# Kernel optimization log

Hardware: AMD Instinct MI355X
Metric: run time of the kernel (lower is better)

## Reference

```python
import jax, jax.numpy as jnp
import numpy as np

L = 3          # num_layers
D = 512        # hidden_dim
B, N = 8, 1024
EPS = 1e-5


def layernorm(x, gamma, beta):
    mu = jnp.mean(x, axis=-1, keepdims=True)
    var = jnp.var(x, axis=-1, keepdims=True)
    return (x - mu) * jax.lax.rsqrt(var + EPS) * gamma + beta


def setup_inputs() -> dict:
    key = jax.random.key(0)
    ks = jax.random.split(key, 12)
    s = 1.0 / np.sqrt(D)
    node_features = jax.random.normal(ks[0], (B, N, D), dtype=jnp.float32)
    adjacency_matrix = jax.random.randint(ks[1], (B, N, N), 0, 2, dtype=jnp.int32)
    return {
        "node_features": node_features,
        "adjacency_matrix": adjacency_matrix,
        # attn_linear: Linear(2D, 1) -> weight [2D], bias scalar, per layer
        "attn_w": jax.random.normal(ks[2], (L, 2 * D), dtype=jnp.float32) * (1.0 / np.sqrt(2 * D)),
        "attn_b": jax.random.normal(ks[3], (L,), dtype=jnp.float32) * 0.01,
        "W1": jax.random.normal(ks[4], (L, D, 4 * D), dtype=jnp.float32) * s,
        "b1": jnp.zeros((L, 4 * D), dtype=jnp.float32),
        "W2": jax.random.normal(ks[5], (L, 4 * D, D), dtype=jnp.float32) * (1.0 / np.sqrt(4 * D)),
        "b2": jnp.zeros((L, D), dtype=jnp.float32),
        "g1": jnp.ones((L, D), dtype=jnp.float32),
        "beta1": jnp.zeros((L, D), dtype=jnp.float32),
        "g2": jnp.ones((L, D), dtype=jnp.float32),
        "beta2": jnp.zeros((L, D), dtype=jnp.float32),
    }


def reference(node_features, adjacency_matrix, attn_w, attn_b, W1, b1, W2, b2, g1, beta1, g2, beta2):
    n = adjacency_matrix.shape[-1]
    # adjacency + self loops; mask of allowed edges
    mask = (adjacency_matrix.astype(jnp.float32) + jnp.eye(n, dtype=jnp.float32)) > 0  # [B,N,N]
    x = node_features
    d = x.shape[-1]
    for l in range(attn_w.shape[0]):
        # score_ij = a1.h_i + a2.h_j + b  (== Linear(concat(h_i,h_j)))
        si = x @ attn_w[l, :d]           # [B,N]
        sj = x @ attn_w[l, d:]           # [B,N]
        scores = si[:, :, None] + sj[:, None, :] + attn_b[l]   # [B,N,N]
        scores = jnp.where(scores >= 0, scores, 0.2 * scores)  # LeakyReLU(0.2)
        scores = jnp.where(mask, scores, -jnp.inf)
        attn = jax.nn.softmax(scores, axis=-1)                  # diag always unmasked
        agg = jnp.einsum('bij,bjd->bid', attn, x)
        h = layernorm(x + agg, g1[l], beta1[l])
        ff = jax.nn.gelu(h @ W1[l] + b1[l], approximate=False) @ W2[l] + b2[l]
        x = layernorm(h + ff, g2[l], beta2[l])
    return x
```

## Files before the change

### kernel.cpp

```cpp
#include <hip/hip_runtime.h>
#include <math.h>

#define NB 8
#define NN 1024
#define DD 512

typedef unsigned short u16;
typedef unsigned int u32;
typedef unsigned long long u64;
typedef __attribute__((ext_vector_type(8))) short bfrag;
typedef __attribute__((ext_vector_type(4))) float ffrag;

__device__ __forceinline__ u16 f2b(float f) {
    union { float f; u32 u; } v; v.f = f;
    u32 r = v.u + 0x7fffu + ((v.u >> 16) & 1u);
    return (u16)(r >> 16);
}
__device__ __forceinline__ float b2f(u16 b) {
    union { u32 u; float f; } v; v.u = ((u32)b) << 16;
    return v.f;
}

__device__ __forceinline__ float gelu_cheap(float v) {
    float s = v * 0.70710678118654752f;
    float a = fabsf(s);
    float t = 1.0f / (1.0f + 0.3275911f * a);
    float p = ((((1.061405429f * t - 1.453152027f) * t + 1.421413741f) * t
                - 0.284496736f) * t + 0.254829592f) * t;
    float erfa = 1.0f - p * __expf(-a * a);
    float erfs = copysignf(erfa, s);
    return 0.5f * v * (1.0f + erfs);
}

__device__ __forceinline__ void gload_lds16(const void* g, void* l) {
    __builtin_amdgcn_global_load_lds(
        (const __attribute__((address_space(1))) void*)g,
        (__attribute__((address_space(3))) void*)l, 16, 0, 0);
}

__device__ __forceinline__ void tcvt_body(
    const float* __restrict__ in, u16* __restrict__ out,
    int R, int C, int r0, int c0, int t, float tile[32][33])
{
    int tr = t >> 3, tc = (t & 7) * 4;
    float4 v = *(const float4*)(in + (size_t)(r0 + tr) * C + c0 + tc);
    tile[tr][tc + 0] = v.x; tile[tr][tc + 1] = v.y;
    tile[tr][tc + 2] = v.z; tile[tr][tc + 3] = v.w;
    __syncthreads();
    u32 w0 = (u32)f2b(tile[tc + 0][tr]) | ((u32)f2b(tile[tc + 1][tr]) << 16);
    u32 w1 = (u32)f2b(tile[tc + 2][tr]) | ((u32)f2b(tile[tc + 3][tr]) << 16);
    uint2 wv; wv.x = w0; wv.y = w1;
    *(uint2*)(out + (size_t)(c0 + tr) * R + r0 + tc) = wv;
}

__global__ __launch_bounds__(256) void transpose_cvt(
    const float* __restrict__ in, u16* __restrict__ out,
    int R, int C, size_t inStr, size_t outStr)
{
    __shared__ float tile[32][33];
    int z = blockIdx.z;
    tcvt_body(in + inStr * z, out + outStr * z,
              R, C, blockIdx.y * 32, blockIdx.x * 32, threadIdx.x, tile);
}

__global__ __launch_bounds__(256) void prep_fused(
    const int* __restrict__ adj, u64* __restrict__ mb,
    const float* __restrict__ nf, const float* __restrict__ attn_w,
    float* __restrict__ si, float* __restrict__ sj, u16* __restrict__ xT)
{
    __shared__ float tile[32][33];
    int bid = blockIdx.x;
    int tid = threadIdx.x;
    if (bid < 512) {
        int idx = bid * 256 + tid;
        int w = idx & 15;
        int bi = idx >> 4;
        int i = bi & 1023;
        const int4* p = (const int4*)(adj + (size_t)bi * NN + w * 64);
        u64 m = 0;
#pragma unroll
        for (int q = 0; q < 16; ++q) {
            int4 v = p[q];
            if (v.x > 0) m |= 1ull << (q * 4 + 0);
            if (v.y > 0) m |= 1ull << (q * 4 + 1);
            if (v.z > 0) m |= 1ull << (q * 4 + 2);
            if (v.w > 0) m |= 1ull << (q * 4 + 3);
        }
        if (w == (i >> 6)) m |= 1ull << (i & 63);
        mb[idx] = m;
    } else if (bid < 2560) {
        int wave = tid >> 6;
        int lane = tid & 63;
        int row = (bid - 512) * 4 + wave;
        const float4* xr = (const float4*)(nf + (size_t)row * DD) + lane * 2;
        const float4* w1 = (const float4*)(attn_w) + lane * 2;
        const float4* w2 = (const float4*)(attn_w + DD) + lane * 2;
        float a = 0.f, b2 = 0.f;
#pragma unroll
        for (int c = 0; c < 2; ++c) {
            float4 xv = xr[c], wa = w1[c], wb = w2[c];
            a  += xv.x * wa.x + xv.y * wa.y + xv.z * wa.z + xv.w * wa.w;
            b2 += xv.x * wb.x + xv.y * wb.y + xv.z * wb.z + xv.w * wb.w;
        }
#pragma unroll
        for (int off = 32; off > 0; off >>= 1) {
            a  += __shfl_xor(a, off);
            b2 += __shfl_xor(b2, off);
        }
        if (lane == 0) { si[row] = a; sj[row] = b2; }
    } else {
        int q = bid - 2560;
        int bx = q & 15, by = (q >> 4) & 31, bz = q >> 9;
        tcvt_body(nf + (size_t)bz * NN * DD, xT + (size_t)bz * NN * DD,
                  1024, 512, by * 32, bx * 32, tid, tile);
    }
}

__global__ __launch_bounds__(256) void trans_w(
    const float* __restrict__ W1, const float* __restrict__ W2,
    u16* __restrict__ W1t, u16* __restrict__ W2t)
{
    __shared__ float tile[32][33];
    int z = blockIdx.z;
    int bx = blockIdx.x, by = blockIdx.y;
    if (z < 3) {
        tcvt_body(W1 + (size_t)z * 512 * 2048, W1t + (size_t)z * 1048576,
                  512, 2048, by * 32, bx * 32, threadIdx.x, tile);
    } else {
        int q = by * 64 + bx;
        int bx2 = q & 15, by2 = q >> 4;
        tcvt_body(W2 + (size_t)(z - 3) * 2048 * 512, W2t + (size_t)(z - 3) * 1048576,
                  2048, 512, by2 * 32, bx2 * 32, threadIdx.x, tile);
    }
}

__global__ __launch_bounds__(256) void softmax_p(
    const float* __restrict__ si, const float* __restrict__ sj,
    const float* __restrict__ attn_b, const u64* __restrict__ mb,
    u16* __restrict__ P)
{
    __shared__ u16 sb[8 * NN];
    int b  = blockIdx.x >> 7;
    int i0 = (blockIdx.x & 127) * 8;
    int tid = threadIdx.x;
    int r = tid >> 5, l32 = tid & 31;
    int i = i0 + r;
    float bb = attn_b[0];
    float siv = si[b * NN + i];
    const float* sjb = sj + b * NN;
    const u64* mbr = mb + ((size_t)b * NN + i) * 16;

    float sv[32];
    float mx = -INFINITY;
#pragma unroll
    for (int q = 0; q < 32; ++q) {
        int j = q * 32 + l32;
        u64 w = mbr[q >> 1];
        int bit = ((q & 1) << 5) + l32;
        float s = siv + sjb[j] + bb;
        s = (s >= 0.f) ? s : 0.2f * s;
        s = ((w >> bit) & 1ull) ? s : -INFINITY;
        sv[q] = s;
        mx = fmaxf(mx, s);
    }
#pragma unroll
    for (int off = 16; off > 0; off >>= 1) mx = fmaxf(mx, __shfl_xor(mx, off, 32));
    float sum = 0.f;
#pragma unroll
    for (int q = 0; q < 32; ++q) {
        float p = __expf(sv[q] - mx);
        sv[q] = p;
        sum += p;
    }
#pragma unroll
    for (int off = 16; off > 0; off >>= 1) sum += __shfl_xor(sum, off, 32);
    float inv = 1.f / sum;
#pragma unroll
    for (int q = 0; q < 32; ++q)
        sb[r * NN + q * 32 + l32] = f2b(sv[q] * inv);
    __syncthreads();
    const uint4* src = (const uint4*)sb;
    uint4* dst = (uint4*)(P + ((size_t)b * NN + i0) * NN);
#pragma unroll
    for (int t = 0; t < 4; ++t) dst[t * 256 + tid] = src[t * 256 + tid];
}

template <int EPI>
__global__ __launch_bounds__(256) void gemm64(
    const u16* __restrict__ A, const u16* __restrict__ Bm,
    const float* __restrict__ bias, const void* __restrict__ res,
    void* __restrict__ Cout, int K, int N, int lda, int ldb,
    size_t aStr, size_t bStr, size_t cStr, size_t resStr)
{
    __shared__ __align__(16) u16 lds[24576];
    int gx = gridDim.x, gy = gridDim.y;
    int wg = blockIdx.x + gx * (blockIdx.y + gy * blockIdx.z);
    int nwg = gx * gy * gridDim.z;
    wg = (wg & 7) * (nwg >> 3) + (wg >> 3);
    int z = wg / (gx * gy);
    int rem = wg - z * (gx * gy);
    int by = rem / gx, bx = rem - by * gx;
    int m0 = by * 64, n0 = bx * 128;
    int tid = threadIdx.x;
    int lane = tid & 63, wv = tid >> 6;

    const u16* ag[2]; const u16* bg[4];
    u32 la[2], lb[4];
#pragma unroll
    for (int i = 0; i < 2; ++i) {
        int q = i * 256 + tid;
        int row = q >> 3, c = q & 7;
        ag[i] = A + aStr * z + (size_t)(m0 + row) * lda + (c ^ (row & 7)) * 8;
        la[i] = i * 2048 + wv * 512;
    }
#pragma unroll
    for (int i = 0; i < 4; ++i) {
        int q = i * 256 + tid;
        int row = q >> 3, c = q & 7;
        bg[i] = Bm + bStr * z + (size_t)(n0 + row) * ldb + (c ^ (row & 7)) * 8;
        lb[i] = 8192 + i * 2048 + wv * 512;
    }

    int mw = (wv >> 1) * 32, nw = (wv & 1) * 64;
    int lr = lane & 15, lq = lane >> 4;
    int sw = lr & 7;

    ffrag acc[2][4];
#pragma unroll
    for (int i = 0; i < 2; ++i)
#pragma unroll
        for (int j = 0; j < 4; ++j) acc[i][j] = (ffrag){0.f, 0.f, 0.f, 0.f};

#pragma unroll
    for (int i = 0; i < 2; ++i) gload_lds16(ag[i], &lds[la[i]]);
#pragma unroll
    for (int i = 0; i < 4; ++i) gload_lds16(bg[i], &lds[lb[i]]);

    for (int k0 = 0; k0 < K; k0 += 64) {
        int cur = (k0 >> 6) & 1;
        if (k0 + 64 < K) {
#pragma unroll
            for (int i = 0; i < 2; ++i)
                gload_lds16(ag[i] + k0 + 64, &lds[((cur ^ 1) << 12) + la[i]]);
#pragma unroll
            for (int i = 0; i < 4; ++i)
                gload_lds16(bg[i] + k0 + 64, &lds[((cur ^ 1) << 13) + lb[i]]);
            asm volatile("s_waitcnt vmcnt(6)" ::: "memory");
        } else {
            asm volatile("s_waitcnt vmcnt(0)" ::: "memory");
        }
        asm volatile("s_barrier" ::: "memory");

        const u16* Ab = &lds[cur << 12];
        const u16* Bb = &lds[8192 + (cur << 13)];
#pragma unroll
        for (int h = 0; h < 2; ++h) {
            bfrag af[2], bf[4];
#pragma unroll
            for (int i = 0; i < 2; ++i)
                af[i] = *(const bfrag*)&Ab[(mw + i * 16 + lr) * 64 + ((h * 4 + lq) ^ sw) * 8];
#pragma unroll
            for (int j = 0; j < 4; ++j)
                bf[j] = *(const bfrag*)&Bb[(nw + j * 16 + lr) * 64 + ((h * 4 + lq) ^ sw) * 8];
#pragma unroll
            for (int i = 0; i < 2; ++i)
#pragma unroll
                for (int j = 0; j < 4; ++j)
                    acc[i][j] = __builtin_amdgcn_mfma_f32_16x16x32_bf16(af[i], bf[j], acc[i][j], 0, 0, 0);
        }
        asm volatile("s_waitcnt lgkmcnt(0)\ns_barrier" ::: "memory");
    }

    float* Cf = (float*)Cout + cStr * z;
    const float* resf = (const float*)res;
    const u16*   resb = (const u16*)res;
#pragma unroll
    for (int i = 0; i < 2; ++i) {
        int row = m0 + mw + i * 16 + lq * 4;
#pragma unroll
        for (int j = 0; j < 4; ++j) {
            int col = n0 + nw + j * 16 + lr;
            float bv = (EPI != 0) ? bias[col] : 0.f;
#pragma unroll
            for (int r = 0; r < 4; ++r) {
                float v = acc[i][j][r] + bv;
                size_t off = (size_t)(row + r) * N + col;
                if (EPI == 0) {
                    Cf[off] = v + resf[resStr * z + off];
                } else {
                    Cf[off] = v + b2f(resb[off]);
                }
            }
        }
    }
}

template <int EPI>
__global__ __launch_bounds__(256) void gemm128(
    const u16* __restrict__ A, const u16* __restrict__ Bm,
    const float* __restrict__ bias, const void* __restrict__ res,
    void* __restrict__ Cout, int K, int N, int lda, int ldb,
    size_t aStr, size_t bStr, size_t cStr, size_t resStr)
{
    __shared__ __align__(16) u16 lds[32768];
    int gx = gridDim.x, gy = gridDim.y;
    int wg = blockIdx.x + gx * (blockIdx.y + gy * blockIdx.z);
    int nwg = gx * gy * gridDim.z;
    wg = (wg & 7) * (nwg >> 3) + (wg >> 3);
    int z = wg / (gx * gy);
    int rem = wg - z * (gx * gy);
    int by = rem / gx, bx = rem - by * gx;
    int m0 = by * 128, n0 = bx * 128;
    int tid = threadIdx.x;
    int lane = tid & 63, wv = tid >> 6;

    const u16* ag[4]; const u16* bg[4];
    u32 la[4], lb[4];
#pragma unroll
    for (int i = 0; i < 4; ++i) {
        int q = i * 256 + tid;
        int row = q >> 3, c = q & 7;
        ag[i] = A + aStr * z + (size_t)(m0 + row) * lda + (c ^ (row & 7)) * 8;
        la[i] = i * 2048 + wv * 512;
        bg[i] = Bm + bStr * z + (size_t)(n0 + row) * ldb + (c ^ (row & 7)) * 8;
        lb[i] = 16384 + i * 2048 + wv * 512;
    }

    int mw = (wv >> 1) * 64, nw = (wv & 1) * 64;
    int lr = lane & 15, lq = lane >> 4;
    int sw = lr & 7;

    ffrag acc[4][4];
#pragma unroll
    for (int i = 0; i < 4; ++i)
#pragma unroll
        for (int j = 0; j < 4; ++j) acc[i][j] = (ffrag){0.f, 0.f, 0.f, 0.f};

#pragma unroll
    for (int i = 0; i < 4; ++i) gload_lds16(ag[i], &lds[la[i]]);
#pragma unroll
    for (int i = 0; i < 4; ++i) gload_lds16(bg[i], &lds[lb[i]]);

    for (int k0 = 0; k0 < K; k0 += 64) {
        int cur = (k0 >> 6) & 1;
        if (k0 + 64 < K) {
#pragma unroll
            for (int i = 0; i < 4; ++i)
                gload_lds16(ag[i] + k0 + 64, &lds[((cur ^ 1) << 13) + la[i]]);
#pragma unroll
            for (int i = 0; i < 4; ++i)
                gload_lds16(bg[i] + k0 + 64, &lds[((cur ^ 1) << 13) + lb[i]]);
            asm volatile("s_waitcnt vmcnt(8)" ::: "memory");
        } else {
            asm volatile("s_waitcnt vmcnt(0)" ::: "memory");
        }
        asm volatile("s_barrier" ::: "memory");

        const u16* Ab = &lds[cur << 13];
        const u16* Bb = &lds[16384 + (cur << 13)];
#pragma unroll
        for (int h = 0; h < 2; ++h) {
            bfrag af[4], bf[4];
#pragma unroll
            for (int i = 0; i < 4; ++i)
                af[i] = *(const bfrag*)&Ab[(mw + i * 16 + lr) * 64 + ((h * 4 + lq) ^ sw) * 8];
#pragma unroll
            for (int j = 0; j < 4; ++j)
                bf[j] = *(const bfrag*)&Bb[(nw + j * 16 + lr) * 64 + ((h * 4 + lq) ^ sw) * 8];
#pragma unroll
            for (int i = 0; i < 4; ++i)
#pragma unroll
                for (int j = 0; j < 4; ++j)
                    acc[i][j] = __builtin_amdgcn_mfma_f32_16x16x32_bf16(af[i], bf[j], acc[i][j], 0, 0, 0);
        }
        asm volatile("s_waitcnt lgkmcnt(0)\ns_barrier" ::: "memory");
    }

    float* Cf = (float*)Cout + cStr * z;
    u16*   Cb = (u16*)Cout + cStr * z;
    const float* resf = (const float*)res;
    const u16*   resb = (const u16*)res;
    if (EPI == 1) {
        u16* sb = lds;
#pragma unroll
        for (int i = 0; i < 4; ++i) {
            int rr = mw + i * 16 + lq * 4;
#pragma unroll
            for (int j = 0; j < 4; ++j) {
                int cc = nw + j * 16 + lr;
                float bv = bias[n0 + cc];
#pragma unroll
                for (int r = 0; r < 4; ++r)
                    sb[(rr + r) * 136 + cc] = f2b(gelu_cheap(acc[i][j][r] + bv));
            }
        }
        __syncthreads();
        u16* Crow = Cb + (size_t)m0 * N + n0;
#pragma unroll
        for (int t = 0; t < 8; ++t) {
            int q = t * 256 + tid;
            int row = q >> 4, c16 = q & 15;
            *(uint4*)(Crow + (size_t)row * N + c16 * 8) =
                *(const uint4*)(sb + row * 136 + c16 * 8);
        }
    } else {
#pragma unroll
        for (int i = 0; i < 4; ++i) {
            int row = m0 + mw + i * 16 + lq * 4;
#pragma unroll
            for (int j = 0; j < 4; ++j) {
                int col = n0 + nw + j * 16 + lr;
                float bv = (EPI != 0) ? bias[col] : 0.f;
#pragma unroll
                for (int r = 0; r < 4; ++r) {
                    float v = acc[i][j][r] + bv;
                    size_t off = (size_t)(row + r) * N + col;
                    if (EPI == 0) {
                        Cf[off] = v + resf[resStr * z + off];
                    } else {
                        Cf[off] = v + b2f(resb[off]);
                    }
                }
            }
        }
    }
}

template <bool BF, bool SP>
__global__ __launch_bounds__(256) void ln_kernel(
    const float* __restrict__ in, const float* __restrict__ g,
    const float* __restrict__ be, void* __restrict__ out,
    const float* __restrict__ aw, float* __restrict__ si, float* __restrict__ sj)
{
    int row = blockIdx.x;
    int tid = threadIdx.x;
    const float2* rp = (const float2*)(in + (size_t)row * DD);
    float2 v = rp[tid];
    float s  = v.x + v.y;
    float ss = v.x * v.x + v.y * v.y;
#pragma unroll
    for (int off = 32; off > 0; off >>= 1) {
        s  += __shfl_xor(s, off);
        ss += __shfl_xor(ss, off);
    }
    __shared__ float sh[8];
    int wave = tid >> 6, lane = tid & 63;
    if (lane == 0) { sh[wave] = s; sh[4 + wave] = ss; }
    __syncthreads();
    float S  = sh[0] + sh[1] + sh[2] + sh[3];
    float SS = sh[4] + sh[5] + sh[6] + sh[7];
    float mean = S * (1.f / DD);
    float var  = SS * (1.f / DD) - mean * mean;
    var = fmaxf(var, 0.f);
    float rs = rsqrtf(var + 1e-5f);
    float2 gv = ((const float2*)g)[tid];
    float2 bv = ((const float2*)be)[tid];
    float ox = (v.x - mean) * rs * gv.x + bv.x;
    float oy = (v.y - mean) * rs * gv.y + bv.y;
    if (BF) {
        u32 w = (u32)f2b(ox) | ((u32)f2b(oy) << 16);
        ((u32*)out)[(size_t)row * (DD / 2) + tid] = w;
    } else {
        float2 o; o.x = ox; o.y = oy;
        ((float2*)out)[(size_t)row * (DD / 2) + tid] = o;
    }
    if (SP) {
        float2 wa = ((const float2*)aw)[tid];
        float2 wb = ((const float2*)(aw + DD))[tid];
        float a = ox * wa.x + oy * wa.y;
        float c = ox * wb.x + oy * wb.y;
#pragma unroll
        for (int off = 32; off > 0; off >>= 1) {
            a += __shfl_xor(a, off);
            c += __shfl_xor(c, off);
        }
        __syncthreads();
        if (lane == 0) { sh[wave] = a; sh[4 + wave] = c; }
        __syncthreads();
        if (tid == 0) {
            si[row] = sh[0] + sh[1] + sh[2] + sh[3];
            sj[row] = sh[4] + sh[5] + sh[6] + sh[7];
        }
    }
}

extern "C" void kernel_launch(void* const* d_in, const int* in_sizes, int n_in,
                              void* d_out, int out_size, void* d_ws, size_t ws_size,
                              hipStream_t stream) {
    const float* nf     = (const float*)d_in[0];
    const int*   adj    = (const int*)d_in[1];
    const float* attn_w = (const float*)d_in[2];
    const float* attn_b = (const float*)d_in[3];
    const float* W1     = (const float*)d_in[4];
    const float* b1     = (const float*)d_in[5];
    const float* W2     = (const float*)d_in[6];
    const float* b2     = (const float*)d_in[7];
    const float* g1     = (const float*)d_in[8];
    const float* be1    = (const float*)d_in[9];
    const float* g2     = (const float*)d_in[10];
    const float* be2    = (const float*)d_in[11];
    float* out = (float*)d_out;

    char* wsb = (char*)d_ws;
    float* x_cur = (float*)(wsb);
    u16*   h_bf  = (u16*)(wsb + 16777216);
    char*  scr   = wsb + 25165824;
    u16*   P     = (u16*)scr;
    float* hres  = (float*)(scr + 16777216);
    u16*   mid   = (u16*)scr;
    u16*   xT    = (u16*)(wsb + 58720256);
    u16*   W1t   = (u16*)(wsb + 67108864);
    u16*   W2t   = (u16*)(wsb + 73400320);
    u64*   mask  = (u64*)(wsb + 79691776);
    float* si    = (float*)(wsb + 80740352);
    float* sj    = (float*)(wsb + 80773120);

    prep_fused<<<6656, 256, 0, stream>>>(adj, mask, nf, attn_w, si, sj, xT);
    trans_w<<<dim3(64, 16, 6), 256, 0, stream>>>(W1, W2, W1t, W2t);

    for (int l = 0; l < 3; ++l) {
        const float* xin = (l == 0) ? nf : x_cur;
        if (l > 0) {
            transpose_cvt<<<dim3(16, 32, 8), 256, 0, stream>>>(xin, xT, 1024, 512,
                                                               (size_t)NN * DD, (size_t)NN * DD);
        }
        softmax_p<<<1024, 256, 0, stream>>>(si, sj, attn_b + l, mask, P);
        gemm64<0><<<dim3(4, 16, 8), 256, 0, stream>>>(
            P, xT, nullptr, xin, hres, 1024, 512, 1024, 1024,
            (size_t)NN * NN, (size_t)DD * NN, (size_t)NN * DD, (size_t)NN * DD);
        ln_kernel<true, false><<<8192, 256, 0, stream>>>(
            hres, g1 + (size_t)l * 512, be1 + (size_t)l * 512, h_bf, nullptr, nullptr, nullptr);
        gemm128<1><<<dim3(16, 64, 1), 256, 0, stream>>>(
            h_bf, W1t + (size_t)l * 1048576, b1 + (size_t)l * 2048, nullptr, mid,
            512, 2048, 512, 512, 0, 0, 0, 0);
        gemm64<2><<<dim3(4, 128, 1), 256, 0, stream>>>(
            mid, W2t + (size_t)l * 1048576, b2 + (size_t)l * 512, h_bf, x_cur,
            2048, 512, 2048, 2048, 0, 0, 0, 0);
        if (l < 2) {
            ln_kernel<false, true><<<8192, 256, 0, stream>>>(
                x_cur, g2 + (size_t)l * 512, be2 + (size_t)l * 512, x_cur,
                attn_w + (size_t)(l + 1) * 1024, si, sj);
        } else {
            ln_kernel<false, false><<<8192, 256, 0, stream>>>(
                x_cur, g2 + (size_t)l * 512, be2 + (size_t)l * 512, out,
                nullptr, nullptr, nullptr);
        }
    }
}
```

Measured before the change: 449.1 us.

## Fuse attention softmax into aggregation GEMM, recomputing probabilities on the fly

Replaces the separate softmax kernel, which wrote a bf16 probability matrix P, and the following P·x GEMM with one kernel. Each workgroup computes row max and sum from si/sj and the adjacency bitmask held in LDS, then builds the bf16 A tile in LDS each k-step and feeds it to MFMA while double-buffering xT tiles. This removes the 16 MB P write and read per layer. The cost is that each of the 4 column-block workgroups per row block recomputes the exponentials, about three passes over the scores.

```diff
diff --git a/kernel.cpp b/kernel.cpp
--- a/kernel.cpp
+++ b/kernel.cpp
@@ -134,55 +134,187 @@
     }
 }
 
-__global__ __launch_bounds__(256) void softmax_p(
+__global__ __launch_bounds__(256) void agg_fused(
     const float* __restrict__ si, const float* __restrict__ sj,
     const float* __restrict__ attn_b, const u64* __restrict__ mb,
-    u16* __restrict__ P)
-{
-    __shared__ u16 sb[8 * NN];
-    int b  = blockIdx.x >> 7;
-    int i0 = (blockIdx.x & 127) * 8;
+    const u16* __restrict__ xT, const float* __restrict__ xres,
+    float* __restrict__ hres)
+{
+    __shared__ __align__(16) u16 ldsB[16384];
+    __shared__ __align__(16) u16 ldsA[4096];
+    __shared__ __align__(16) float sjl[1024];
+    __shared__ __align__(16) u64 ml[1024];
+
+    int gx = gridDim.x, gy = gridDim.y;
+    int wg = blockIdx.x + gx * (blockIdx.y + gy * blockIdx.z);
+    int nwg = gx * gy * gridDim.z;
+    wg = (wg & 7) * (nwg >> 3) + (wg >> 3);
+    int z = wg / (gx * gy);
+    int rem = wg - z * (gx * gy);
+    int by = rem / gx, bx = rem - by * gx;
+    int m0 = by * 64, n0 = bx * 128;
     int tid = threadIdx.x;
-    int r = tid >> 5, l32 = tid & 31;
-    int i = i0 + r;
+    int lane = tid & 63, wv = tid >> 6;
+
+    const u16* bg[4];
+    u32 lbB[4];
+#pragma unroll
+    for (int i = 0; i < 4; ++i) {
+        int q = i * 256 + tid;
+        int row = q >> 3, c = q & 7;
+        bg[i] = xT + (size_t)z * DD * NN + (size_t)(n0 + row) * NN + (c ^ (row & 7)) * 8;
+        lbB[i] = i * 4096 + wv * 1024;
+    }
+
+    gload_lds16((const char*)(sj + (size_t)z * NN) + (size_t)tid * 16,
+                (char*)sjl + wv * 1024);
+    {
+        const char* mg = (const char*)(mb + ((size_t)z * NN + m0) * 16);
+#pragma unroll
+        for (int i = 0; i < 2; ++i)
+            gload_lds16(mg + (size_t)(i * 256 + tid) * 16,
+                        (char*)ml + i * 4096 + wv * 1024);
+    }
+#pragma unroll
+    for (int i = 0; i < 4; ++i)
+        gload_lds16(bg[i], (char*)ldsB + lbB[i]);
+    asm volatile("s_waitcnt vmcnt(0)" ::: "memory");
+    __syncthreads();
+
     float bb = attn_b[0];
-    float siv = si[b * NN + i];
-    const float* sjb = sj + b * NN;
-    const u64* mbr = mb + ((size_t)b * NN + i) * 16;
-
-    float sv[32];
+    int prow = tid >> 2, pq = tid & 3;
+    float siv = si[(size_t)z * NN + m0 + prow];
+    const u64* mrow = &ml[prow * 16];
     float mx = -INFINITY;
 #pragma unroll
-    for (int q = 0; q < 32; ++q) {
-        int j = q * 32 + l32;
-        u64 w = mbr[q >> 1];
-        int bit = ((q & 1) << 5) + l32;
-        float s = siv + sjb[j] + bb;
-        s = (s >= 0.f) ? s : 0.2f * s;
-        s = ((w >> bit) & 1ull) ? s : -INFINITY;
-        sv[q] = s;
-        mx = fmaxf(mx, s);
-    }
-#pragma unroll
-    for (int off = 16; off > 0; off >>= 1) mx = fmaxf(mx, __shfl_xor(mx, off, 32));
+    for (int g = 0; g < 4; ++g) {
+        u64 w = mrow[pq * 4 + g];
+        const float4* s4 = (const float4*)(sjl + pq * 256 + g * 64);
+#pragma unroll 4
+        for (int k = 0; k < 16; ++k) {
+            float4 v = s4[k];
+            float s0 = siv + v.x + bb; s0 = s0 >= 0.f ? s0 : 0.2f * s0;
+            float s1 = siv + v.y + bb; s1 = s1 >= 0.f ? s1 : 0.2f * s1;
+            float s2 = siv + v.z + bb; s2 = s2 >= 0.f ? s2 : 0.2f * s2;
+            float s3 = siv + v.w + bb; s3 = s3 >= 0.f ? s3 : 0.2f * s3;
+            int b0 = k * 4;
+            if (!((w >> (b0 + 0)) & 1ull)) s0 = -INFINITY;
+            if (!((w >> (b0 + 1)) & 1ull)) s1 = -INFINITY;
+            if (!((w >> (b0 + 2)) & 1ull)) s2 = -INFINITY;
+            if (!((w >> (b0 + 3)) & 1ull)) s3 = -INFINITY;
+            mx = fmaxf(mx, fmaxf(fmaxf(s0, s1), fmaxf(s2, s3)));
+        }
+    }
+    mx = fmaxf(mx, __shfl_xor(mx, 1));
+    mx = fmaxf(mx, __shfl_xor(mx, 2));
     float sum = 0.f;
 #pragma unroll
-    for (int q = 0; q < 32; ++q) {
-        float p = __expf(sv[q] - mx);
-        sv[q] = p;
-        sum += p;
-    }
-#pragma unroll
-    for (int off = 16; off > 0; off >>= 1) sum += __shfl_xor(sum, off, 32);
+    for (int g = 0; g < 4; ++g) {
+        u64 w = mrow[pq * 4 + g];
+        const float4* s4 = (const float4*)(sjl + pq * 256 + g * 64);
+#pragma unroll 4
+        for (int k = 0; k < 16; ++k) {
+            float4 v = s4[k];
+            float s0 = siv + v.x + bb; s0 = s0 >= 0.f ? s0 : 0.2f * s0;
+            float s1 = siv + v.y + bb; s1 = s1 >= 0.f ? s1 : 0.2f * s1;
+            float s2 = siv + v.z + bb; s2 = s2 >= 0.f ? s2 : 0.2f * s2;
+            float s3 = siv + v.w + bb; s3 = s3 >= 0.f ? s3 : 0.2f * s3;
+            int b0 = k * 4;
+            if (!((w >> (b0 + 0)) & 1ull)) s0 = -INFINITY;
+            if (!((w >> (b0 + 1)) & 1ull)) s1 = -INFINITY;
+            if (!((w >> (b0 + 2)) & 1ull)) s2 = -INFINITY;
+            if (!((w >> (b0 + 3)) & 1ull)) s3 = -INFINITY;
+            sum += __expf(s0 - mx) + __expf(s1 - mx)
+                 + __expf(s2 - mx) + __expf(s3 - mx);
+        }
+    }
+    sum += __shfl_xor(sum, 1);
+    sum += __shfl_xor(sum, 2);
     float inv = 1.f / sum;
-#pragma unroll
-    for (int q = 0; q < 32; ++q)
-        sb[r * NN + q * 32 + l32] = f2b(sv[q] * inv);
-    __syncthreads();
-    const uint4* src = (const uint4*)sb;
-    uint4* dst = (uint4*)(P + ((size_t)b * NN + i0) * NN);
-#pragma unroll
-    for (int t = 0; t < 4; ++t) dst[t * 256 + tid] = src[t * 256 + tid];
+
+    int mw = (wv >> 1) * 32, nw = (wv & 1) * 64;
+    int lr = lane & 15, lq = lane >> 4;
+    int sw = lr & 7;
+    int rsw7 = prow & 7;
+    int jj16 = pq * 16;
+    u32* a32 = (u32*)ldsA;
+
+    ffrag acc[2][4];
+#pragma unroll
+    for (int i = 0; i < 2; ++i)
+#pragma unroll
+        for (int j = 0; j < 4; ++j) acc[i][j] = (ffrag){0.f, 0.f, 0.f, 0.f};
+
+    for (int t = 0; t < 16; ++t) {
+        if (t + 1 < 16) {
+#pragma unroll
+            for (int i = 0; i < 4; ++i)
+                gload_lds16(bg[i] + (t + 1) * 64,
+                            (char*)ldsB + ((t + 1) & 1) * 16384 + lbB[i]);
+        }
+        {
+            u64 w = mrow[t];
+            const float4* s4 = (const float4*)(sjl + t * 64 + jj16);
+#pragma unroll
+            for (int k4 = 0; k4 < 4; ++k4) {
+                float4 v = s4[k4];
+                int kk = jj16 + k4 * 4;
+                float s0 = siv + v.x + bb; s0 = s0 >= 0.f ? s0 : 0.2f * s0;
+                float s1 = siv + v.y + bb; s1 = s1 >= 0.f ? s1 : 0.2f * s1;
+                float s2 = siv + v.z + bb; s2 = s2 >= 0.f ? s2 : 0.2f * s2;
+                float s3 = siv + v.w + bb; s3 = s3 >= 0.f ? s3 : 0.2f * s3;
+                float p0 = ((w >> (kk + 0)) & 1ull) ? __expf(s0 - mx) * inv : 0.f;
+                float p1 = ((w >> (kk + 1)) & 1ull) ? __expf(s1 - mx) * inv : 0.f;
+                float p2 = ((w >> (kk + 2)) & 1ull) ? __expf(s2 - mx) * inv : 0.f;
+                float p3 = ((w >> (kk + 3)) & 1ull) ? __expf(s3 - mx) * inv : 0.f;
+                u32 lo = (u32)f2b(p0) | ((u32)f2b(p1) << 16);
+                u32 hi = (u32)f2b(p2) | ((u32)f2b(p3) << 16);
+                int off = prow * 64 + (((kk >> 3) ^ rsw7) << 3) + (kk & 7);
+                a32[off >> 1] = lo;
+                a32[(off >> 1) + 1] = hi;
+            }
+        }
+        if (t + 1 < 16) {
+            asm volatile("s_waitcnt vmcnt(4) lgkmcnt(0)" ::: "memory");
+        } else {
+            asm volatile("s_waitcnt vmcnt(0) lgkmcnt(0)" ::: "memory");
+        }
+        asm volatile("s_barrier" ::: "memory");
+
+        const u16* Bb = &ldsB[(t & 1) * 8192];
+#pragma unroll
+        for (int h = 0; h < 2; ++h) {
+            bfrag af[2], bf[4];
+#pragma unroll
+            for (int i = 0; i < 2; ++i)
+                af[i] = *(const bfrag*)&ldsA[(mw + i * 16 + lr) * 64 + ((h * 4 + lq) ^ sw) * 8];
+#pragma unroll
+            for (int j = 0; j < 4; ++j)
+                bf[j] = *(const bfrag*)&Bb[(nw + j * 16 + lr) * 64 + ((h * 4 + lq) ^ sw) * 8];
+#pragma unroll
+            for (int i = 0; i < 2; ++i)
+#pragma unroll
+                for (int j = 0; j < 4; ++j)
+                    acc[i][j] = __builtin_amdgcn_mfma_f32_16x16x32_bf16(af[i], bf[j], acc[i][j], 0, 0, 0);
+        }
+        asm volatile("s_waitcnt lgkmcnt(0)\ns_barrier" ::: "memory");
+    }
+
+    float* Cf = hres + (size_t)z * NN * DD;
+    const float* rf = xres + (size_t)z * NN * DD;
+#pragma unroll
+    for (int i = 0; i < 2; ++i) {
+        int row = m0 + mw + i * 16 + lq * 4;
+#pragma unroll
+        for (int j = 0; j < 4; ++j) {
+            int col = n0 + nw + j * 16 + lr;
+#pragma unroll
+            for (int r = 0; r < 4; ++r) {
+                size_t off = (size_t)(row + r) * DD + col;
+                Cf[off] = acc[i][j][r] + rf[off];
+            }
+        }
+    }
 }
 
 template <int EPI>
@@ -505,7 +637,6 @@
     float* x_cur = (float*)(wsb);
     u16*   h_bf  = (u16*)(wsb + 16777216);
     char*  scr   = wsb + 25165824;
-    u16*   P     = (u16*)scr;
     float* hres  = (float*)(scr + 16777216);
     u16*   mid   = (u16*)scr;
     u16*   xT    = (u16*)(wsb + 58720256);
@@ -524,10 +655,8 @@
             transpose_cvt<<<dim3(16, 32, 8), 256, 0, stream>>>(xin, xT, 1024, 512,
                                                                (size_t)NN * DD, (size_t)NN * DD);
         }
-        softmax_p<<<1024, 256, 0, stream>>>(si, sj, attn_b + l, mask, P);
-        gemm64<0><<<dim3(4, 16, 8), 256, 0, stream>>>(
-            P, xT, nullptr, xin, hres, 1024, 512, 1024, 1024,
-            (size_t)NN * NN, (size_t)DD * NN, (size_t)NN * DD, (size_t)NN * DD);
+        agg_fused<<<dim3(4, 16, 8), 256, 0, stream>>>(
+            si, sj, attn_b + l, mask, xT, xin, hres);
         ln_kernel<true, false><<<8192, 256, 0, stream>>>(
             hres, g1 + (size_t)l * 512, be1 + (size_t)l * 512, h_bf, nullptr, nullptr, nullptr);
         gemm128<1><<<dim3(16, 64, 1), 256, 0, stream>>>(
```

New measurement: 526.1 us. 1.17x slower.
